# Kernel tuning notes

Hardware: AMD Instinct MI355X
Metric: run time of the kernel (lower is better)

The kernel has to match this reference:

```python
import jax, jax.numpy as jnp
import numpy as np

N = 100000      # nodes
K = 16          # neighbors per node
C_IN = 16
C1 = 64
C2 = 128
C_OUT = 40


def setup_inputs() -> dict:
    key = jax.random.key(0)
    ks = jax.random.split(key, 12)
    x = jax.random.normal(ks[0], (N, C_IN), dtype=jnp.float32)
    # kNN-style edge list: row = arange(N) repeated K times, col = neighbor ids
    row = jnp.repeat(jnp.arange(N, dtype=jnp.int32), K)
    col = jax.random.randint(ks[1], (N * K,), 0, N, dtype=jnp.int32)
    edge_index = jnp.stack([row, col], axis=0)  # [2, E]
    s = 0.02
    params = {
        'W1': jax.random.normal(ks[2], (2 * C_IN, C1), jnp.float32) * s,
        'b1': jnp.zeros((C1,), jnp.float32),
        'W2': jax.random.normal(ks[3], (C1, C1), jnp.float32) * s,
        'b2': jnp.zeros((C1,), jnp.float32),
        'W3': jax.random.normal(ks[4], (2 * C1, C2), jnp.float32) * s,
        'b3': jnp.zeros((C2,), jnp.float32),
        'W4': jax.random.normal(ks[5], (C2, C2), jnp.float32) * s,
        'b4': jnp.zeros((C2,), jnp.float32),
        'W5': jax.random.normal(ks[6], (C2, C2), jnp.float32) * s,
        'b5': jnp.zeros((C2,), jnp.float32),
        'W6': jax.random.normal(ks[7], (C2, C_OUT), jnp.float32) * s,
        'b6': jnp.zeros((C_OUT,), jnp.float32),
    }
    return {'x': x, 'edge_index': edge_index, **params}


def _edge_conv(x, row, col, Wa, ba, Wb, bb):
    # gather + diff + concat: [E, 2*C]
    xr = x[row]
    e = jnp.concatenate([xr, x[col] - xr], axis=-1)
    h = jax.nn.relu(e @ Wa + ba)
    return jax.nn.relu(h @ Wb + bb)


def reference(x, edge_index, W1, b1, W2, b2, W3, b3, W4, b4, W5, b5, W6, b6):
    row, col = edge_index[0], edge_index[1]
    h1 = _edge_conv(x, row, col, W1, b1, W2, b2)      # [E, 64]
    # as in the source, conv2 indexes the edge-feature tensor with node ids
    h2 = _edge_conv(h1, row, col, W3, b3, W4, b4)     # [E, 128]
    # max over the K neighbors of each node (edges grouped by row node)
    g = h2.reshape(N, K, C2).max(axis=1)              # [N, 128]
    out = jax.nn.relu(g @ W5 + b5) @ W6 + b6          # [N, out]
    return out
```

## Files before the change

### kernel.cpp

```cpp
#include <hip/hip_runtime.h>


#define NN 100000
#define KNB 16
#define EE (NN * KNB)

#define W2F 0
#define W3F 8
#define W4F 40
#define W5F 72
#define W6F 104
#define NFRAG 116

typedef float floatx4 __attribute__((ext_vector_type(4)));
typedef __bf16 bf16x8 __attribute__((ext_vector_type(8)));

static __device__ __forceinline__ unsigned f2bf_rne_u(float f) {
    unsigned u = __float_as_uint(f);
    return (u + 0x7FFFu + ((u >> 16) & 1u)) >> 16;
}
static __device__ __forceinline__ float bfu2f(unsigned h) {
    return __uint_as_float(h << 16);
}

static __device__ __forceinline__ void split_pack2(float a, float b,
                                                   unsigned& hp, unsigned& lp) {
    unsigned ua = __float_as_uint(a), ub = __float_as_uint(b);
    hp = __builtin_amdgcn_perm(ub, ua, 0x07060302u);
    float ra = a - __uint_as_float(ua & 0xFFFF0000u);
    float rb = b - __uint_as_float(ub & 0xFFFF0000u);
    unsigned la = __float_as_uint(ra), lb = __float_as_uint(rb);
    la = la + 0x7FFFu + ((la >> 16) & 1u);
    lb = lb + 0x7FFFu + ((lb >> 16) & 1u);
    lp = __builtin_amdgcn_perm(lb, la, 0x07060302u);
}

static __device__ __forceinline__ void split8(float4 f0, float4 f1,
                                              bf16x8& ah, bf16x8& al) {
    unsigned hd[4], ld[4];
    split_pack2(f0.x, f0.y, hd[0], ld[0]);
    split_pack2(f0.z, f0.w, hd[1], ld[1]);
    split_pack2(f1.x, f1.y, hd[2], ld[2]);
    split_pack2(f1.z, f1.w, hd[3], ld[3]);
    uint4 H = {hd[0], hd[1], hd[2], hd[3]};
    uint4 L = {ld[0], ld[1], ld[2], ld[3]};
    ah = __builtin_bit_cast(bf16x8, H);
    al = __builtin_bit_cast(bf16x8, L);
}

__global__ __launch_bounds__(256) void kw_kernel(
    const float* __restrict__ W2, const float* __restrict__ W3,
    const float* __restrict__ W4, const float* __restrict__ W5,
    const float* __restrict__ W6,
    unsigned short* __restrict__ WH, unsigned short* __restrict__ WL)
{
    int d = blockIdx.x * 256 + threadIdx.x;
    if (d >= NFRAG * 64) return;
    int f = d >> 6, l = d & 63, c = l & 15, q = l >> 4;
    float v[8];
    if (f < W3F) {
        int fx = f - W2F, kc = fx >> 2, nt = fx & 3;
        int k0 = kc * 32 + q * 8, n = nt * 16 + c;
#pragma unroll
        for (int j = 0; j < 8; ++j) v[j] = W2[(k0 + j) * 64 + n];
    } else if (f < W4F) {
        int fx = f - W3F, kc = fx >> 4, nt = fx & 15;
        int k0 = kc * 32 + q * 8, n = nt * 16 + c;
#pragma unroll
        for (int j = 0; j < 8; ++j) {
            int k = k0 + j;
            v[j] = (n < 128) ? (W3[k * 128 + n] - W3[(64 + k) * 128 + n])
                             : W3[(64 + k) * 128 + (n - 128)];
        }
    } else if (f < W5F) {
        int fx = f - W4F, kc = fx >> 3, nt = fx & 7;
        int k0 = kc * 32 + q * 8, n = nt * 16 + c;
#pragma unroll
        for (int j = 0; j < 8; ++j) v[j] = W4[(k0 + j) * 128 + n];
    } else if (f < W6F) {
        int fx = f - W5F, kc = fx >> 3, nt = fx & 7;
        int k0 = kc * 32 + q * 8, n = nt * 16 + c;
#pragma unroll
        for (int j = 0; j < 8; ++j) v[j] = W5[(k0 + j) * 128 + n];
    } else {
        int fx = f - W6F, kc = fx / 3, nt = fx % 3;
        int k0 = kc * 32 + q * 8, n = nt * 16 + c;
#pragma unroll
        for (int j = 0; j < 8; ++j)
            v[j] = (n < 40) ? W6[(k0 + j) * 40 + n] : 0.0f;
    }
    unsigned hs[8], ls[8];
#pragma unroll
    for (int j = 0; j < 8; ++j) {
        unsigned h = f2bf_rne_u(v[j]);
        float r = v[j] - bfu2f(h);
        hs[j] = h;
        ls[j] = f2bf_rne_u(r);
    }
    uint4 H, L;
    H.x = hs[0] | (hs[1] << 16); H.y = hs[2] | (hs[3] << 16);
    H.z = hs[4] | (hs[5] << 16); H.w = hs[6] | (hs[7] << 16);
    L.x = ls[0] | (ls[1] << 16); L.y = ls[2] | (ls[3] << 16);
    L.z = ls[4] | (ls[5] << 16); L.w = ls[6] | (ls[7] << 16);
    *(uint4*)(WH + (size_t)d * 8) = H;
    *(uint4*)(WL + (size_t)d * 8) = L;
}

__global__ __launch_bounds__(256) void k1_kernel(
    const float* __restrict__ x, const float* __restrict__ W1,
    const float* __restrict__ b1, float* __restrict__ A1, float* __restrict__ B1)
{
    int gid = blockIdx.x * 256 + threadIdx.x;
    int n = gid >> 6;
    int j = gid & 63;
    const float* xr = x + n * 16;
    float acc_a = b1[j];
    float acc_b = 0.0f;
#pragma unroll
    for (int k = 0; k < 16; ++k) {
        float xv = xr[k];
        float wt = W1[k * 64 + j];
        float wb = W1[(16 + k) * 64 + j];
        acc_a = fmaf(xv, wt - wb, acc_a);
        acc_b = fmaf(xv, wb, acc_b);
    }
    A1[n * 64 + j] = acc_a;
    B1[n * 64 + j] = acc_b;
}

__global__ __launch_bounds__(256) void k2_kernel(
    const int* __restrict__ col,
    const float* __restrict__ A1, const float* __restrict__ B1,
    const unsigned short* __restrict__ WH, const unsigned short* __restrict__ WL,
    const float* __restrict__ b2, const float* __restrict__ b3,
    float* __restrict__ A3, float* __restrict__ B3)
{
    __shared__ __align__(16) float tF[8 * 512];
    __shared__ __align__(16) float hF[8 * 512];
    const int t = threadIdx.x;
    const int i0 = blockIdx.x * 64;

    {
        const int row = t & 63, part = t >> 6;
        int i = i0 + row;
        int nn = i >> 4;
        int ci = col[i];
        const float* ar = A1 + (size_t)nn * 64 + part * 16;
        const float* br = B1 + (size_t)ci * 64 + part * 16;
        int mt = row >> 4, m = row & 15, kc = part >> 1;
        float* base = tF + (mt * 2 + kc) * 512 + m * 8;
#pragma unroll
        for (int h = 0; h < 2; ++h) {
            int qq = (part & 1) * 2 + h;
            float4 a0 = *(const float4*)(ar + h * 8);
            float4 b0 = *(const float4*)(br + h * 8);
            float4 a1 = *(const float4*)(ar + h * 8 + 4);
            float4 b1v = *(const float4*)(br + h * 8 + 4);
            float4 r0, r1;
            r0.x = fmaxf(a0.x + b0.x, 0.0f); r0.y = fmaxf(a0.y + b0.y, 0.0f);
            r0.z = fmaxf(a0.z + b0.z, 0.0f); r0.w = fmaxf(a0.w + b0.w, 0.0f);
            r1.x = fmaxf(a1.x + b1v.x, 0.0f); r1.y = fmaxf(a1.y + b1v.y, 0.0f);
            r1.z = fmaxf(a1.z + b1v.z, 0.0f); r1.w = fmaxf(a1.w + b1v.w, 0.0f);
            *(float4*)(base + qq * 128) = r0;
            *(float4*)(base + qq * 128 + 4) = r1;
        }
    }
    __syncthreads();

    const int w = __builtin_amdgcn_readfirstlane(t >> 6);
    const int lane = t & 63;

    floatx4 acc1[4];
#pragma unroll
    for (int nt = 0; nt < 4; ++nt) acc1[nt] = (floatx4){0.f, 0.f, 0.f, 0.f};
#pragma unroll
    for (int kc = 0; kc < 2; ++kc) {
        const float* ap = tF + (w * 2 + kc) * 512 + lane * 8;
        bf16x8 ah, al;
        split8(*(const float4*)ap, *(const float4*)(ap + 4), ah, al);
#pragma unroll
        for (int nt = 0; nt < 4; ++nt) {
            size_t fb = (size_t)(W2F + kc * 4 + nt) * 512 + lane * 8;
            bf16x8 bh = __builtin_bit_cast(bf16x8, *(const uint4*)(WH + fb));
            bf16x8 bl = __builtin_bit_cast(bf16x8, *(const uint4*)(WL + fb));
            acc1[nt] = __builtin_amdgcn_mfma_f32_16x16x32_bf16(ah, bh, acc1[nt], 0, 0, 0);
            acc1[nt] = __builtin_amdgcn_mfma_f32_16x16x32_bf16(ah, bl, acc1[nt], 0, 0, 0);
            acc1[nt] = __builtin_amdgcn_mfma_f32_16x16x32_bf16(al, bh, acc1[nt], 0, 0, 0);
        }
    }
    {
        const int qq = lane >> 4, cc = lane & 15;
#pragma unroll
        for (int nt = 0; nt < 4; ++nt) {
            float bv = b2[nt * 16 + cc];
            int colIdx = nt * 16 + cc;
            int kc2 = colIdx >> 5, q2 = (colIdx >> 3) & 3, jj = cc & 7;
            float* dst = hF + (w * 2 + kc2) * 512 + q2 * 128 + jj;
#pragma unroll
            for (int r = 0; r < 4; ++r)
                dst[(qq * 4 + r) * 8] = fmaxf(acc1[nt][r] + bv, 0.0f);
        }
    }
    floatx4 acc2[16];
#pragma unroll
    for (int nt = 0; nt < 16; ++nt) acc2[nt] = (floatx4){0.f, 0.f, 0.f, 0.f};
#pragma unroll
    for (int kc = 0; kc < 2; ++kc) {
        const float* ap = hF + (w * 2 + kc) * 512 + lane * 8;
        bf16x8 ah, al;
        split8(*(const float4*)ap, *(const float4*)(ap + 4), ah, al);
#pragma unroll
        for (int nt = 0; nt < 16; ++nt) {
            size_t fb = (size_t)(W3F + kc * 16 + nt) * 512 + lane * 8;
            bf16x8 bh = __builtin_bit_cast(bf16x8, *(const uint4*)(WH + fb));
            bf16x8 bl = __builtin_bit_cast(bf16x8, *(const uint4*)(WL + fb));
            acc2[nt] = __builtin_amdgcn_mfma_f32_16x16x32_bf16(ah, bh, acc2[nt], 0, 0, 0);
            acc2[nt] = __builtin_amdgcn_mfma_f32_16x16x32_bf16(ah, bl, acc2[nt], 0, 0, 0);
            acc2[nt] = __builtin_amdgcn_mfma_f32_16x16x32_bf16(al, bh, acc2[nt], 0, 0, 0);
        }
    }
    {
        const int qq = lane >> 4, cc = lane & 15;
#pragma unroll
        for (int nt = 0; nt < 16; ++nt) {
            int n = nt * 16 + cc;
            float bv = (n < 128) ? b3[n] : 0.0f;
#pragma unroll
            for (int r = 0; r < 4; ++r) {
                int i = i0 + w * 16 + qq * 4 + r;
                if (i < NN) {
                    float vv = acc2[nt][r];
                    if (n < 128) A3[(size_t)i * 128 + n] = vv + bv;
                    else         B3[(size_t)i * 128 + (n - 128)] = vv;
                }
            }
        }
    }
}

__global__ __launch_bounds__(256, 2) void k3_kernel(
    const int* __restrict__ col,
    const float* __restrict__ A3, const float* __restrict__ B3,
    const unsigned short* __restrict__ WH, const unsigned short* __restrict__ WL,
    const float* __restrict__ b4, const float* __restrict__ b5,
    const float* __restrict__ b6, float* __restrict__ out)
{
    __shared__ __align__(16) unsigned short wlds[16384];
    __shared__ __align__(16) float ashare[2048];
    __shared__ __align__(16) float gshare[2048];
    const int t = threadIdx.x;
    const int lane = t & 63;
    const int w = t >> 6;
    const int m = lane & 15, q = lane >> 4;
    const int nodeB = blockIdx.x * 16;
    const int node0 = nodeB + w * 4;

    float4 braw[16];
#pragma unroll
    for (int ng = 0; ng < 2; ++ng) {
        const int c = col[(node0 + ng) * KNB + m];
        const float* br = B3 + (size_t)c * 128 + q * 8;
#pragma unroll
        for (int kc = 0; kc < 4; ++kc) {
            braw[ng * 8 + kc * 2]     = *(const float4*)(br + kc * 32);
            braw[ng * 8 + kc * 2 + 1] = *(const float4*)(br + kc * 32 + 4);
        }
    }
    {
        const float4* asrc = (const float4*)(A3 + (size_t)nodeB * 128);
        float4* adst = (float4*)ashare;
        adst[t]       = asrc[t];
        adst[t + 256] = asrc[t + 256];
        const uint4* hsrc = (const uint4*)(WH + (size_t)W4F * 512);
        uint4* wdst = (uint4*)wlds;
#pragma unroll
        for (int i = 0; i < 8; ++i) wdst[t + i * 256] = hsrc[t + i * 256];
    }
    __syncthreads();

    const unsigned short* wlo = WL + (size_t)W4F * 512 + lane * 8;

#pragma unroll
    for (int p = 0; p < 2; ++p) {
        bf16x8 aH[2][4], aL[2][4];
#pragma unroll
        for (int ng = 0; ng < 2; ++ng) {
            const float* ar = ashare + (w * 4 + p * 2 + ng) * 128 + q * 8;
#pragma unroll
            for (int kc = 0; kc < 4; ++kc) {
                float4 b0 = braw[ng * 8 + kc * 2];
                float4 b1 = braw[ng * 8 + kc * 2 + 1];
                float4 a0 = *(const float4*)(ar + kc * 32);
                float4 a1 = *(const float4*)(ar + kc * 32 + 4);
                float v0 = fmaxf(a0.x + b0.x, 0.0f), v1 = fmaxf(a0.y + b0.y, 0.0f);
                float v2 = fmaxf(a0.z + b0.z, 0.0f), v3 = fmaxf(a0.w + b0.w, 0.0f);
                float v4 = fmaxf(a1.x + b1.x, 0.0f), v5 = fmaxf(a1.y + b1.y, 0.0f);
                float v6 = fmaxf(a1.z + b1.z, 0.0f), v7 = fmaxf(a1.w + b1.w, 0.0f);
                uint4 H, L;
                split_pack2(v0, v1, H.x, L.x);
                split_pack2(v2, v3, H.y, L.y);
                split_pack2(v4, v5, H.z, L.z);
                split_pack2(v6, v7, H.w, L.w);
                aH[ng][kc] = __builtin_bit_cast(bf16x8, H);
                aL[ng][kc] = __builtin_bit_cast(bf16x8, L);
            }
        }
        if (p == 0) {
#pragma unroll
            for (int ng = 0; ng < 2; ++ng) {
                const int c = col[(node0 + 2 + ng) * KNB + m];
                const float* br = B3 + (size_t)c * 128 + q * 8;
#pragma unroll
                for (int kc = 0; kc < 4; ++kc) {
                    braw[ng * 8 + kc * 2]     = *(const float4*)(br + kc * 32);
                    braw[ng * 8 + kc * 2 + 1] = *(const float4*)(br + kc * 32 + 4);
                }
            }
        }
        floatx4 acc[2][8];
#pragma unroll
        for (int ng = 0; ng < 2; ++ng)
#pragma unroll
            for (int nt = 0; nt < 8; ++nt)
                acc[ng][nt] = (floatx4){0.0f, 0.0f, 0.0f, 0.0f};
#pragma unroll
        for (int kc = 0; kc < 4; ++kc) {
#pragma unroll
            for (int nt = 0; nt < 8; ++nt) {
                const int f = kc * 8 + nt;
                bf16x8 bh = __builtin_bit_cast(bf16x8,
                    *(const uint4*)(wlds + f * 512 + lane * 8));
                bf16x8 bl = __builtin_bit_cast(bf16x8,
                    *(const uint4*)(wlo + (size_t)f * 512));
#pragma unroll
                for (int ng = 0; ng < 2; ++ng) {
                    acc[ng][nt] = __builtin_amdgcn_mfma_f32_16x16x32_bf16(
                        aH[ng][kc], bh, acc[ng][nt], 0, 0, 0);
                    acc[ng][nt] = __builtin_amdgcn_mfma_f32_16x16x32_bf16(
                        aH[ng][kc], bl, acc[ng][nt], 0, 0, 0);
                    acc[ng][nt] = __builtin_amdgcn_mfma_f32_16x16x32_bf16(
                        aL[ng][kc], bh, acc[ng][nt], 0, 0, 0);
                }
            }
        }
#pragma unroll
        for (int ng = 0; ng < 2; ++ng) {
            const int mloc = w * 4 + p * 2 + ng;
#pragma unroll
            for (int nt = 0; nt < 8; ++nt) {
                floatx4 a = acc[ng][nt];
                float mm = fmaxf(fmaxf(a[0], a[1]), fmaxf(a[2], a[3]));
                mm = fmaxf(mm, __shfl_xor(mm, 16));
                mm = fmaxf(mm, __shfl_xor(mm, 32));
                if (lane < 16) {
                    int colI = nt * 16 + lane;
                    int kc2 = colI >> 5, q2 = (colI >> 3) & 3, jj = colI & 7;
                    gshare[kc2 * 512 + q2 * 128 + mloc * 8 + jj] =
                        fmaxf(mm + b4[colI], 0.0f);
                }
            }
        }
    }

    __syncthreads();
    floatx4 acc5[2];
    acc5[0] = (floatx4){0.f, 0.f, 0.f, 0.f};
    acc5[1] = (floatx4){0.f, 0.f, 0.f, 0.f};
#pragma unroll
    for (int kc = 0; kc < 4; ++kc) {
        const float* ap = gshare + kc * 512 + lane * 8;
        bf16x8 ah, al;
        split8(*(const float4*)ap, *(const float4*)(ap + 4), ah, al);
#pragma unroll
        for (int ntl = 0; ntl < 2; ++ntl) {
            int nt = w * 2 + ntl;
            size_t fb = (size_t)(W5F + kc * 8 + nt) * 512 + lane * 8;
            bf16x8 bh = __builtin_bit_cast(bf16x8, *(const uint4*)(WH + fb));
            bf16x8 bl = __builtin_bit_cast(bf16x8, *(const uint4*)(WL + fb));
            acc5[ntl] = __builtin_amdgcn_mfma_f32_16x16x32_bf16(ah, bh, acc5[ntl], 0, 0, 0);
            acc5[ntl] = __builtin_amdgcn_mfma_f32_16x16x32_bf16(ah, bl, acc5[ntl], 0, 0, 0);
            acc5[ntl] = __builtin_amdgcn_mfma_f32_16x16x32_bf16(al, bh, acc5[ntl], 0, 0, 0);
        }
    }
    {
        const int qq = lane >> 4, cc = lane & 15;
#pragma unroll
        for (int ntl = 0; ntl < 2; ++ntl) {
            int nt = w * 2 + ntl;
            float bv = b5[nt * 16 + cc];
            int colI = nt * 16 + cc;
            int kc2 = colI >> 5, q2 = (colI >> 3) & 3, jj = cc & 7;
            float* dst = ashare + kc2 * 512 + q2 * 128 + jj;
#pragma unroll
            for (int r = 0; r < 4; ++r)
                dst[(qq * 4 + r) * 8] = fmaxf(acc5[ntl][r] + bv, 0.0f);
        }
    }
    __syncthreads();
    if (w < 3) {
        floatx4 acc6 = (floatx4){0.f, 0.f, 0.f, 0.f};
#pragma unroll
        for (int kc = 0; kc < 4; ++kc) {
            const float* ap = ashare + kc * 512 + lane * 8;
            bf16x8 ah, al;
            split8(*(const float4*)ap, *(const float4*)(ap + 4), ah, al);
            size_t fb = (size_t)(W6F + kc * 3 + w) * 512 + lane * 8;
            bf16x8 bh = __builtin_bit_cast(bf16x8, *(const uint4*)(WH + fb));
            bf16x8 bl = __builtin_bit_cast(bf16x8, *(const uint4*)(WL + fb));
            acc6 = __builtin_amdgcn_mfma_f32_16x16x32_bf16(ah, bh, acc6, 0, 0, 0);
            acc6 = __builtin_amdgcn_mfma_f32_16x16x32_bf16(ah, bl, acc6, 0, 0, 0);
            acc6 = __builtin_amdgcn_mfma_f32_16x16x32_bf16(al, bh, acc6, 0, 0, 0);
        }
        const int qq = lane >> 4, cc = lane & 15;
        int n = w * 16 + cc;
        if (n < 40) {
            float bv = b6[n];
#pragma unroll
            for (int r = 0; r < 4; ++r)
                out[(size_t)(nodeB + qq * 4 + r) * 40 + n] = acc6[r] + bv;
        }
    }
}

extern "C" void kernel_launch(void* const* d_in, const int* in_sizes, int n_in,
                              void* d_out, int out_size, void* d_ws, size_t ws_size,
                              hipStream_t stream)
{
    const float* x  = (const float*)d_in[0];
    const int* ei   = (const int*)d_in[1];
    const int* col  = ei + EE;
    const float* W1 = (const float*)d_in[2];
    const float* b1 = (const float*)d_in[3];
    const float* W2 = (const float*)d_in[4];
    const float* b2 = (const float*)d_in[5];
    const float* W3 = (const float*)d_in[6];
    const float* b3 = (const float*)d_in[7];
    const float* W4 = (const float*)d_in[8];
    const float* b4 = (const float*)d_in[9];
    const float* W5 = (const float*)d_in[10];
    const float* b5 = (const float*)d_in[11];
    const float* W6 = (const float*)d_in[12];
    const float* b6 = (const float*)d_in[13];
    float* out = (float*)d_out;

    float* A1 = (float*)d_ws;
    float* B1 = A1 + (size_t)NN * 64;
    float* A3 = B1 + (size_t)NN * 64;
    float* B3 = A3 + (size_t)NN * 128;
    unsigned short* WH = (unsigned short*)(B3 + (size_t)NN * 128);
    unsigned short* WL = WH + NFRAG * 512;

    kw_kernel<<<(NFRAG * 64 + 255) / 256, 256, 0, stream>>>(W2, W3, W4, W5, W6, WH, WL);
    k1_kernel<<<NN * 64 / 256, 256, 0, stream>>>(x, W1, b1, A1, B1);
    k2_kernel<<<(NN + 63) / 64, 256, 0, stream>>>(col, A1, B1, WH, WL, b2, b3, A3, B3);
    k3_kernel<<<NN / 16, 256, 0, stream>>>(col, A3, B3, WH, WL, b4, b5, b6, out);
}
```

Before: 480.0 us.

## Split k3 B3 gather into K-halves to cut registers and raise occupancy

```diff
diff --git a/kernel.cpp b/kernel.cpp
--- a/kernel.cpp
+++ b/kernel.cpp
@@ -238,7 +238,7 @@
     }
 }
 
-__global__ __launch_bounds__(256, 2) void k3_kernel(
+__global__ __launch_bounds__(256, 3) void k3_kernel(
     const int* __restrict__ col,
     const float* __restrict__ A3, const float* __restrict__ B3,
     const unsigned short* __restrict__ WH, const unsigned short* __restrict__ WL,
@@ -255,15 +255,15 @@
     const int nodeB = blockIdx.x * 16;
     const int node0 = nodeB + w * 4;
 
-    float4 braw[16];
+    float4 brawA[8], brawB[8];
 #pragma unroll
     for (int ng = 0; ng < 2; ++ng) {
         const int c = col[(node0 + ng) * KNB + m];
         const float* br = B3 + (size_t)c * 128 + q * 8;
 #pragma unroll
-        for (int kc = 0; kc < 4; ++kc) {
-            braw[ng * 8 + kc * 2]     = *(const float4*)(br + kc * 32);
-            braw[ng * 8 + kc * 2 + 1] = *(const float4*)(br + kc * 32 + 4);
+        for (int kk = 0; kk < 2; ++kk) {
+            brawA[ng * 4 + kk * 2]     = *(const float4*)(br + kk * 32);
+            brawA[ng * 4 + kk * 2 + 1] = *(const float4*)(br + kk * 32 + 4);
         }
     }
     {
@@ -282,16 +282,34 @@
 
 #pragma unroll
     for (int p = 0; p < 2; ++p) {
-        bf16x8 aH[2][4], aL[2][4];
+        floatx4 acc[2][8];
+#pragma unroll
+        for (int ng = 0; ng < 2; ++ng)
+#pragma unroll
+            for (int nt = 0; nt < 8; ++nt)
+                acc[ng][nt] = (floatx4){0.0f, 0.0f, 0.0f, 0.0f};
+
+#pragma unroll
+        for (int ng = 0; ng < 2; ++ng) {
+            const int c = col[(node0 + p * 2 + ng) * KNB + m];
+            const float* br = B3 + (size_t)c * 128 + q * 8;
+#pragma unroll
+            for (int kk = 0; kk < 2; ++kk) {
+                brawB[ng * 4 + kk * 2]     = *(const float4*)(br + (2 + kk) * 32);
+                brawB[ng * 4 + kk * 2 + 1] = *(const float4*)(br + (2 + kk) * 32 + 4);
+            }
+        }
+
+        bf16x8 aH[2][2], aL[2][2];
 #pragma unroll
         for (int ng = 0; ng < 2; ++ng) {
             const float* ar = ashare + (w * 4 + p * 2 + ng) * 128 + q * 8;
 #pragma unroll
-            for (int kc = 0; kc < 4; ++kc) {
-                float4 b0 = braw[ng * 8 + kc * 2];
-                float4 b1 = braw[ng * 8 + kc * 2 + 1];
-                float4 a0 = *(const float4*)(ar + kc * 32);
-                float4 a1 = *(const float4*)(ar + kc * 32 + 4);
+            for (int kk = 0; kk < 2; ++kk) {
+                float4 b0 = brawA[ng * 4 + kk * 2];
+                float4 b1 = brawA[ng * 4 + kk * 2 + 1];
+                float4 a0 = *(const float4*)(ar + kk * 32);
+                float4 a1 = *(const float4*)(ar + kk * 32 + 4);
                 float v0 = fmaxf(a0.x + b0.x, 0.0f), v1 = fmaxf(a0.y + b0.y, 0.0f);
                 float v2 = fmaxf(a0.z + b0.z, 0.0f), v3 = fmaxf(a0.w + b0.w, 0.0f);
                 float v4 = fmaxf(a1.x + b1.x, 0.0f), v5 = fmaxf(a1.y + b1.y, 0.0f);
@@ -301,33 +319,15 @@
                 split_pack2(v2, v3, H.y, L.y);
                 split_pack2(v4, v5, H.z, L.z);
                 split_pack2(v6, v7, H.w, L.w);
-                aH[ng][kc] = __builtin_bit_cast(bf16x8, H);
-                aL[ng][kc] = __builtin_bit_cast(bf16x8, L);
-            }
-        }
-        if (p == 0) {
-#pragma unroll
-            for (int ng = 0; ng < 2; ++ng) {
-                const int c = col[(node0 + 2 + ng) * KNB + m];
-                const float* br = B3 + (size_t)c * 128 + q * 8;
-#pragma unroll
-                for (int kc = 0; kc < 4; ++kc) {
-                    braw[ng * 8 + kc * 2]     = *(const float4*)(br + kc * 32);
-                    braw[ng * 8 + kc * 2 + 1] = *(const float4*)(br + kc * 32 + 4);
-                }
-            }
-        }
-        floatx4 acc[2][8];
-#pragma unroll
-        for (int ng = 0; ng < 2; ++ng)
-#pragma unroll
-            for (int nt = 0; nt < 8; ++nt)
-                acc[ng][nt] = (floatx4){0.0f, 0.0f, 0.0f, 0.0f};
-#pragma unroll
-        for (int kc = 0; kc < 4; ++kc) {
+                aH[ng][kk] = __builtin_bit_cast(bf16x8, H);
+                aL[ng][kk] = __builtin_bit_cast(bf16x8, L);
+            }
+        }
+#pragma unroll
+        for (int kk = 0; kk < 2; ++kk) {
 #pragma unroll
             for (int nt = 0; nt < 8; ++nt) {
-                const int f = kc * 8 + nt;
+                const int f = kk * 8 + nt;
                 bf16x8 bh = __builtin_bit_cast(bf16x8,
                     *(const uint4*)(wlds + f * 512 + lane * 8));
                 bf16x8 bl = __builtin_bit_cast(bf16x8,
@@ -335,14 +335,71 @@
 #pragma unroll
                 for (int ng = 0; ng < 2; ++ng) {
                     acc[ng][nt] = __builtin_amdgcn_mfma_f32_16x16x32_bf16(
-                        aH[ng][kc], bh, acc[ng][nt], 0, 0, 0);
+                        aH[ng][kk], bh, acc[ng][nt], 0, 0, 0);
                     acc[ng][nt] = __builtin_amdgcn_mfma_f32_16x16x32_bf16(
-                        aH[ng][kc], bl, acc[ng][nt], 0, 0, 0);
+                        aH[ng][kk], bl, acc[ng][nt], 0, 0, 0);
                     acc[ng][nt] = __builtin_amdgcn_mfma_f32_16x16x32_bf16(
-                        aL[ng][kc], bh, acc[ng][nt], 0, 0, 0);
+                        aL[ng][kk], bh, acc[ng][nt], 0, 0, 0);
                 }
             }
         }
+
+        if (p == 0) {
+#pragma unroll
+            for (int ng = 0; ng < 2; ++ng) {
+                const int c = col[(node0 + 2 + ng) * KNB + m];
+                const float* br = B3 + (size_t)c * 128 + q * 8;
+#pragma unroll
+                for (int kk = 0; kk < 2; ++kk) {
+                    brawA[ng * 4 + kk * 2]     = *(const float4*)(br + kk * 32);
+                    brawA[ng * 4 + kk * 2 + 1] = *(const float4*)(br + kk * 32 + 4);
+                }
+            }
+        }
+
+#pragma unroll
+        for (int ng = 0; ng < 2; ++ng) {
+            const float* ar = ashare + (w * 4 + p * 2 + ng) * 128 + q * 8;
+#pragma unroll
+            for (int kk = 0; kk < 2; ++kk) {
+                float4 b0 = brawB[ng * 4 + kk * 2];
+                float4 b1 = brawB[ng * 4 + kk * 2 + 1];
+                float4 a0 = *(const float4*)(ar + (2 + kk) * 32);
+                float4 a1 = *(const float4*)(ar + (2 + kk) * 32 + 4);
+                float v0 = fmaxf(a0.x + b0.x, 0.0f), v1 = fmaxf(a0.y + b0.y, 0.0f);
+                float v2 = fmaxf(a0.z + b0.z, 0.0f), v3 = fmaxf(a0.w + b0.w, 0.0f);
+                float v4 = fmaxf(a1.x + b1.x, 0.0f), v5 = fmaxf(a1.y + b1.y, 0.0f);
+                float v6 = fmaxf(a1.z + b1.z, 0.0f), v7 = fmaxf(a1.w + b1.w, 0.0f);
+                uint4 H, L;
+                split_pack2(v0, v1, H.x, L.x);
+                split_pack2(v2, v3, H.y, L.y);
+                split_pack2(v4, v5, H.z, L.z);
+                split_pack2(v6, v7, H.w, L.w);
+                aH[ng][kk] = __builtin_bit_cast(bf16x8, H);
+                aL[ng][kk] = __builtin_bit_cast(bf16x8, L);
+            }
+        }
+#pragma unroll
+        for (int kk = 0; kk < 2; ++kk) {
+#pragma unroll
+            for (int nt = 0; nt < 8; ++nt) {
+                const int f = (2 + kk) * 8 + nt;
+                bf16x8 bh = __builtin_bit_cast(bf16x8,
+                    *(const uint4*)(wlds + f * 512 + lane * 8));
+                bf16x8 bl = __builtin_bit_cast(bf16x8,
+                    *(const uint4*)(wlo + (size_t)f * 512));
+#pragma unroll
+                for (int ng = 0; ng < 2; ++ng) {
+                    acc[ng][nt] = __builtin_amdgcn_mfma_f32_16x16x32_bf16(
+                        aH[ng][kk], bh, acc[ng][nt], 0, 0, 0);
+                    acc[ng][nt] = __builtin_amdgcn_mfma_f32_16x16x32_bf16(
+                        aH[ng][kk], bl, acc[ng][nt], 0, 0, 0);
+                    acc[ng][nt] = __builtin_amdgcn_mfma_f32_16x16x32_bf16(
+                        aL[ng][kk], bh, acc[ng][nt], 0, 0, 0);
+                }
+            }
+        }
+
 #pragma unroll
         for (int ng = 0; ng < 2; ++ng) {
             const int mloc = w * 4 + p * 2 + ng;
```

Result: no change. 471.0 us (-1.9%).

## Gather 64-wide H1 rows and recompute B3 projection inside k3

Applied to the files above, without the earlier changes.

```diff
diff --git a/kernel.cpp b/kernel.cpp
--- a/kernel.cpp
+++ b/kernel.cpp
@@ -133,7 +133,7 @@
     const float* __restrict__ A1, const float* __restrict__ B1,
     const unsigned short* __restrict__ WH, const unsigned short* __restrict__ WL,
     const float* __restrict__ b2, const float* __restrict__ b3,
-    float* __restrict__ A3, float* __restrict__ B3)
+    float* __restrict__ A3, float* __restrict__ H1)
 {
     __shared__ __align__(16) float tF[8 * 512];
     __shared__ __align__(16) float hF[8 * 512];
@@ -197,20 +197,24 @@
             int kc2 = colIdx >> 5, q2 = (colIdx >> 3) & 3, jj = cc & 7;
             float* dst = hF + (w * 2 + kc2) * 512 + q2 * 128 + jj;
 #pragma unroll
-            for (int r = 0; r < 4; ++r)
-                dst[(qq * 4 + r) * 8] = fmaxf(acc1[nt][r] + bv, 0.0f);
-        }
-    }
-    floatx4 acc2[16];
-#pragma unroll
-    for (int nt = 0; nt < 16; ++nt) acc2[nt] = (floatx4){0.f, 0.f, 0.f, 0.f};
+            for (int r = 0; r < 4; ++r) {
+                float hv = fmaxf(acc1[nt][r] + bv, 0.0f);
+                dst[(qq * 4 + r) * 8] = hv;
+                int i = i0 + w * 16 + qq * 4 + r;
+                if (i < NN) H1[(size_t)i * 64 + colIdx] = hv;
+            }
+        }
+    }
+    floatx4 acc2[8];
+#pragma unroll
+    for (int nt = 0; nt < 8; ++nt) acc2[nt] = (floatx4){0.f, 0.f, 0.f, 0.f};
 #pragma unroll
     for (int kc = 0; kc < 2; ++kc) {
         const float* ap = hF + (w * 2 + kc) * 512 + lane * 8;
         bf16x8 ah, al;
         split8(*(const float4*)ap, *(const float4*)(ap + 4), ah, al);
 #pragma unroll
-        for (int nt = 0; nt < 16; ++nt) {
+        for (int nt = 0; nt < 8; ++nt) {
             size_t fb = (size_t)(W3F + kc * 16 + nt) * 512 + lane * 8;
             bf16x8 bh = __builtin_bit_cast(bf16x8, *(const uint4*)(WH + fb));
             bf16x8 bl = __builtin_bit_cast(bf16x8, *(const uint4*)(WL + fb));
@@ -222,17 +226,13 @@
     {
         const int qq = lane >> 4, cc = lane & 15;
 #pragma unroll
-        for (int nt = 0; nt < 16; ++nt) {
+        for (int nt = 0; nt < 8; ++nt) {
             int n = nt * 16 + cc;
-            float bv = (n < 128) ? b3[n] : 0.0f;
+            float bv = b3[n];
 #pragma unroll
             for (int r = 0; r < 4; ++r) {
                 int i = i0 + w * 16 + qq * 4 + r;
-                if (i < NN) {
-                    float vv = acc2[nt][r];
-                    if (n < 128) A3[(size_t)i * 128 + n] = vv + bv;
-                    else         B3[(size_t)i * 128 + (n - 128)] = vv;
-                }
+                if (i < NN) A3[(size_t)i * 128 + n] = acc2[nt][r] + bv;
             }
         }
     }
@@ -240,12 +240,13 @@
 
 __global__ __launch_bounds__(256, 2) void k3_kernel(
     const int* __restrict__ col,
-    const float* __restrict__ A3, const float* __restrict__ B3,
+    const float* __restrict__ A3, const float* __restrict__ H1,
     const unsigned short* __restrict__ WH, const unsigned short* __restrict__ WL,
     const float* __restrict__ b4, const float* __restrict__ b5,
     const float* __restrict__ b6, float* __restrict__ out)
 {
     __shared__ __align__(16) unsigned short wlds[16384];
+    __shared__ __align__(16) float escratch[8192];
     __shared__ __align__(16) float ashare[2048];
     __shared__ __align__(16) float gshare[2048];
     const int t = threadIdx.x;
@@ -255,22 +256,21 @@
     const int nodeB = blockIdx.x * 16;
     const int node0 = nodeB + w * 4;
 
-    float4 braw[16];
+    float4 hA[8], hB[8];
 #pragma unroll
     for (int ng = 0; ng < 2; ++ng) {
         const int c = col[(node0 + ng) * KNB + m];
-        const float* br = B3 + (size_t)c * 128 + q * 8;
-#pragma unroll
-        for (int kc = 0; kc < 4; ++kc) {
-            braw[ng * 8 + kc * 2]     = *(const float4*)(br + kc * 32);
-            braw[ng * 8 + kc * 2 + 1] = *(const float4*)(br + kc * 32 + 4);
-        }
+        const float* hr = H1 + (size_t)c * 64 + q * 8;
+        hA[ng * 4 + 0] = *(const float4*)(hr);
+        hA[ng * 4 + 1] = *(const float4*)(hr + 4);
+        hA[ng * 4 + 2] = *(const float4*)(hr + 32);
+        hA[ng * 4 + 3] = *(const float4*)(hr + 36);
     }
     {
-        const float4* asrc = (const float4*)(A3 + (size_t)nodeB * 128);
-        float4* adst = (float4*)ashare;
-        adst[t]       = asrc[t];
-        adst[t + 256] = asrc[t + 256];
+        const floatx4* asrc = (const floatx4*)(A3 + (size_t)nodeB * 128);
+        floatx4* adst = (floatx4*)ashare;
+        adst[t]       = __builtin_nontemporal_load(asrc + t);
+        adst[t + 256] = __builtin_nontemporal_load(asrc + t + 256);
         const uint4* hsrc = (const uint4*)(WH + (size_t)W4F * 512);
         uint4* wdst = (uint4*)wlds;
 #pragma unroll
@@ -279,42 +279,19 @@
     __syncthreads();
 
     const unsigned short* wlo = WL + (size_t)W4F * 512 + lane * 8;
+    float* escr = escratch + w * 2048;
 
 #pragma unroll
     for (int p = 0; p < 2; ++p) {
-        bf16x8 aH[2][4], aL[2][4];
-#pragma unroll
-        for (int ng = 0; ng < 2; ++ng) {
-            const float* ar = ashare + (w * 4 + p * 2 + ng) * 128 + q * 8;
-#pragma unroll
-            for (int kc = 0; kc < 4; ++kc) {
-                float4 b0 = braw[ng * 8 + kc * 2];
-                float4 b1 = braw[ng * 8 + kc * 2 + 1];
-                float4 a0 = *(const float4*)(ar + kc * 32);
-                float4 a1 = *(const float4*)(ar + kc * 32 + 4);
-                float v0 = fmaxf(a0.x + b0.x, 0.0f), v1 = fmaxf(a0.y + b0.y, 0.0f);
-                float v2 = fmaxf(a0.z + b0.z, 0.0f), v3 = fmaxf(a0.w + b0.w, 0.0f);
-                float v4 = fmaxf(a1.x + b1.x, 0.0f), v5 = fmaxf(a1.y + b1.y, 0.0f);
-                float v6 = fmaxf(a1.z + b1.z, 0.0f), v7 = fmaxf(a1.w + b1.w, 0.0f);
-                uint4 H, L;
-                split_pack2(v0, v1, H.x, L.x);
-                split_pack2(v2, v3, H.y, L.y);
-                split_pack2(v4, v5, H.z, L.z);
-                split_pack2(v6, v7, H.w, L.w);
-                aH[ng][kc] = __builtin_bit_cast(bf16x8, H);
-                aL[ng][kc] = __builtin_bit_cast(bf16x8, L);
-            }
-        }
         if (p == 0) {
 #pragma unroll
             for (int ng = 0; ng < 2; ++ng) {
                 const int c = col[(node0 + 2 + ng) * KNB + m];
-                const float* br = B3 + (size_t)c * 128 + q * 8;
-#pragma unroll
-                for (int kc = 0; kc < 4; ++kc) {
-                    braw[ng * 8 + kc * 2]     = *(const float4*)(br + kc * 32);
-                    braw[ng * 8 + kc * 2 + 1] = *(const float4*)(br + kc * 32 + 4);
-                }
+                const float* hr = H1 + (size_t)c * 64 + q * 8;
+                hB[ng * 4 + 0] = *(const float4*)(hr);
+                hB[ng * 4 + 1] = *(const float4*)(hr + 4);
+                hB[ng * 4 + 2] = *(const float4*)(hr + 32);
+                hB[ng * 4 + 3] = *(const float4*)(hr + 36);
             }
         }
         floatx4 acc[2][8];
@@ -323,26 +300,83 @@
 #pragma unroll
             for (int nt = 0; nt < 8; ++nt)
                 acc[ng][nt] = (floatx4){0.0f, 0.0f, 0.0f, 0.0f};
-#pragma unroll
-        for (int kc = 0; kc < 4; ++kc) {
-#pragma unroll
-            for (int nt = 0; nt < 8; ++nt) {
-                const int f = kc * 8 + nt;
-                bf16x8 bh = __builtin_bit_cast(bf16x8,
-                    *(const uint4*)(wlds + f * 512 + lane * 8));
-                bf16x8 bl = __builtin_bit_cast(bf16x8,
-                    *(const uint4*)(wlo + (size_t)f * 512));
+
+#pragma unroll
+        for (int h = 0; h < 2; ++h) {
+            floatx4 b3acc[2][4];
+#pragma unroll
+            for (int ng = 0; ng < 2; ++ng)
+#pragma unroll
+                for (int nt = 0; nt < 4; ++nt)
+                    b3acc[ng][nt] = (floatx4){0.0f, 0.0f, 0.0f, 0.0f};
+#pragma unroll
+            for (int kc = 0; kc < 2; ++kc) {
+                bf16x8 ah[2], al[2];
 #pragma unroll
                 for (int ng = 0; ng < 2; ++ng) {
-                    acc[ng][nt] = __builtin_amdgcn_mfma_f32_16x16x32_bf16(
-                        aH[ng][kc], bh, acc[ng][nt], 0, 0, 0);
-                    acc[ng][nt] = __builtin_amdgcn_mfma_f32_16x16x32_bf16(
-                        aH[ng][kc], bl, acc[ng][nt], 0, 0, 0);
-                    acc[ng][nt] = __builtin_amdgcn_mfma_f32_16x16x32_bf16(
-                        aL[ng][kc], bh, acc[ng][nt], 0, 0, 0);
-                }
-            }
-        }
+                    float4 h0 = (p == 0) ? hA[ng * 4 + kc * 2]     : hB[ng * 4 + kc * 2];
+                    float4 h1v = (p == 0) ? hA[ng * 4 + kc * 2 + 1] : hB[ng * 4 + kc * 2 + 1];
+                    split8(h0, h1v, ah[ng], al[ng]);
+                }
+#pragma unroll
+                for (int nt = 0; nt < 4; ++nt) {
+                    size_t fb = (size_t)(W3F + kc * 16 + 8 + h * 4 + nt) * 512 + lane * 8;
+                    bf16x8 bh = __builtin_bit_cast(bf16x8, *(const uint4*)(WH + fb));
+                    bf16x8 bl = __builtin_bit_cast(bf16x8, *(const uint4*)(WL + fb));
+#pragma unroll
+                    for (int ng = 0; ng < 2; ++ng) {
+                        b3acc[ng][nt] = __builtin_amdgcn_mfma_f32_16x16x32_bf16(
+                            ah[ng], bh, b3acc[ng][nt], 0, 0, 0);
+                        b3acc[ng][nt] = __builtin_amdgcn_mfma_f32_16x16x32_bf16(
+                            ah[ng], bl, b3acc[ng][nt], 0, 0, 0);
+                        b3acc[ng][nt] = __builtin_amdgcn_mfma_f32_16x16x32_bf16(
+                            al[ng], bh, b3acc[ng][nt], 0, 0, 0);
+                    }
+                }
+            }
+#pragma unroll
+            for (int ng = 0; ng < 2; ++ng) {
+                const int node_l = w * 4 + p * 2 + ng;
+#pragma unroll
+                for (int nt = 0; nt < 4; ++nt) {
+                    const int c = h * 64 + nt * 16 + m;
+                    float a3v = ashare[node_l * 128 + c];
+                    float* eb = escr + ng * 1024 + (nt >> 1) * 512
+                              + ((nt * 2 + (m >> 3)) & 3) * 128 + (m & 7);
+#pragma unroll
+                    for (int r = 0; r < 4; ++r)
+                        eb[(q * 4 + r) * 8] = fmaxf(a3v + b3acc[ng][nt][r], 0.0f);
+                }
+            }
+#pragma unroll
+            for (int kk = 0; kk < 2; ++kk) {
+                const int kc2 = h * 2 + kk;
+                bf16x8 aH[2], aL[2];
+#pragma unroll
+                for (int ng = 0; ng < 2; ++ng) {
+                    const float* ap = escr + ng * 1024 + kk * 512 + lane * 8;
+                    split8(*(const float4*)ap, *(const float4*)(ap + 4), aH[ng], aL[ng]);
+                }
+#pragma unroll
+                for (int nt = 0; nt < 8; ++nt) {
+                    const int f = kc2 * 8 + nt;
+                    bf16x8 bh = __builtin_bit_cast(bf16x8,
+                        *(const uint4*)(wlds + f * 512 + lane * 8));
+                    bf16x8 bl = __builtin_bit_cast(bf16x8,
+                        *(const uint4*)(wlo + (size_t)f * 512));
+#pragma unroll
+                    for (int ng = 0; ng < 2; ++ng) {
+                        acc[ng][nt] = __builtin_amdgcn_mfma_f32_16x16x32_bf16(
+                            aH[ng], bh, acc[ng][nt], 0, 0, 0);
+                        acc[ng][nt] = __builtin_amdgcn_mfma_f32_16x16x32_bf16(
+                            aH[ng], bl, acc[ng][nt], 0, 0, 0);
+                        acc[ng][nt] = __builtin_amdgcn_mfma_f32_16x16x32_bf16(
+                            aL[ng], bh, acc[ng][nt], 0, 0, 0);
+                    }
+                }
+            }
+        }
+
 #pragma unroll
         for (int ng = 0; ng < 2; ++ng) {
             const int mloc = w * 4 + p * 2 + ng;
@@ -446,12 +480,12 @@
     float* A1 = (float*)d_ws;
     float* B1 = A1 + (size_t)NN * 64;
     float* A3 = B1 + (size_t)NN * 64;
-    float* B3 = A3 + (size_t)NN * 128;
-    unsigned short* WH = (unsigned short*)(B3 + (size_t)NN * 128);
+    float* H1 = A3 + (size_t)NN * 128;
+    unsigned short* WH = (unsigned short*)(H1 + (size_t)NN * 128);
     unsigned short* WL = WH + NFRAG * 512;
 
     kw_kernel<<<(NFRAG * 64 + 255) / 256, 256, 0, stream>>>(W2, W3, W4, W5, W6, WH, WL);
     k1_kernel<<<NN * 64 / 256, 256, 0, stream>>>(x, W1, b1, A1, B1);
-    k2_kernel<<<(NN + 63) / 64, 256, 0, stream>>>(col, A1, B1, WH, WL, b2, b3, A3, B3);
-    k3_kernel<<<NN / 16, 256, 0, stream>>>(col, A3, B3, WH, WL, b4, b5, b6, out);
-}
+    k2_kernel<<<(NN + 63) / 64, 256, 0, stream>>>(col, A1, B1, WH, WL, b2, b3, A3, H1);
+    k3_kernel<<<NN / 16, 256, 0, stream>>>(col, A3, H1, WH, WL, b4, b5, b6, out);
+}
```

Result: slower. 495.2 us (+3.2%).
